# Optimization experiments

Hardware: AMD Instinct MI355X
Metric: run time of the kernel (lower is better)

The kernel has to match this reference:

```python
import jax, jax.numpy as jnp
import numpy as np


def _cross_head_proj(x, sw, qw1, qw2, kw1, kw2, qdd, kdd):
    # x: [B,N,T,S] attention logits/probs; sw: [N,N]
    # qw1/qw2: [B,T,I,N], kw1/kw2: [B,S,I,N] (I=2 dynamic rank), qdd: [B,T,N], kdd: [B,S,N]
    out = x + jnp.einsum('bnts,nm->bmts', x, sw)
    # low-rank dynamic mixing along query positions (sum over i reproduces the range(2) loop)
    qh = jnp.einsum('bnts,btin->bits', x, qw1)          # [B,I,T,S]
    out = out + jnp.einsum('bits,btin->bnts', qh, qw2)
    # low-rank dynamic mixing along key positions
    kh = jnp.einsum('bnts,bsin->bits', x, kw1)          # [B,I,T,S]
    out = out + jnp.einsum('bits,bsin->bnts', kh, kw2)
    # diagonal (per-head) dynamic terms
    out = out + x * jnp.transpose(qdd, (0, 2, 1))[:, :, :, None]   # [B,N,T,1]
    out = out + x * jnp.transpose(kdd, (0, 2, 1))[:, :, None, :]   # [B,N,1,S]
    return out


def setup_inputs() -> dict:
    key = jax.random.key(0)
    ks = jax.random.split(key, 18)
    B, N, T, S, D, I = 1, 32, 1024, 1024, 128, 2
    scale = 0.05  # dynamic weights come out of tanh/RMSnorm in the original; keep them small
    query = jax.random.normal(ks[0], (B, N, T, D), jnp.float32) * (D ** -0.5)
    k_ = jax.random.normal(ks[1], (B, N, S, D), jnp.float32)
    v_ = jax.random.normal(ks[2], (B, N, S, D), jnp.float32)
    neg = jnp.finfo(jnp.float32).min * 0.5  # matches make_causal_mask
    atten_mask = jnp.where(jnp.arange(S)[None, :] <= jnp.arange(T)[:, None], 0.0, neg).astype(jnp.float32)
    def dws(i0):
        return (
            jax.random.normal(ks[i0 + 0], (N, N), jnp.float32) * scale,
            jax.random.normal(ks[i0 + 1], (B, T, I, N), jnp.float32) * scale,
            jax.random.normal(ks[i0 + 2], (B, T, I, N), jnp.float32) * scale,
            jax.random.normal(ks[i0 + 3], (B, S, I, N), jnp.float32) * scale,
            jax.random.normal(ks[i0 + 4], (B, S, I, N), jnp.float32) * scale,
            jax.random.normal(ks[i0 + 5], (B, T, N), jnp.float32) * scale,
            jax.random.normal(ks[i0 + 6], (B, S, N), jnp.float32) * scale,
        )
    sw_pre, qw1_pre, qw2_pre, kw1_pre, kw2_pre, qdd_pre, kdd_pre = dws(3)
    sw_post, qw1_post, qw2_post, kw1_post, kw2_post, qdd_post, kdd_post = dws(10)
    return {
        'query': query, 'key': k_, 'value': v_, 'atten_mask': atten_mask,
        'sw_pre': sw_pre, 'qw1_pre': qw1_pre, 'qw2_pre': qw2_pre, 'kw1_pre': kw1_pre,
        'kw2_pre': kw2_pre, 'qdd_pre': qdd_pre, 'kdd_pre': kdd_pre,
        'sw_post': sw_post, 'qw1_post': qw1_post, 'qw2_post': qw2_post, 'kw1_post': kw1_post,
        'kw2_post': kw2_post, 'qdd_post': qdd_post, 'kdd_post': kdd_post,
    }


def reference(query, key, value, atten_mask,
              sw_pre, qw1_pre, qw2_pre, kw1_pre, kw2_pre, qdd_pre, kdd_pre,
              sw_post, qw1_post, qw2_post, kw1_post, kw2_post, qdd_post, kdd_post):
    # _atten_context: QK^T -> pre cross-head proj -> mask -> softmax -> post cross-head proj -> AV
    logits = jnp.einsum('bntd,bnsd->bnts', query, key)
    logits = _cross_head_proj(logits, sw_pre, qw1_pre, qw2_pre, kw1_pre, kw2_pre, qdd_pre, kdd_pre)
    logits = logits + atten_mask  # [T,S] broadcasts over [B,N,T,S]
    probs = jax.nn.softmax(logits, axis=-1)
    probs = _cross_head_proj(probs, sw_post, qw1_post, qw2_post, kw1_post, kw2_post, qdd_post, kdd_post)
    return jnp.einsum('bnts,bnsd->bntd', probs, value)
```

## Files before the change

kernel.cpp:

```cpp
#include <hip/hip_runtime.h>
#include <hip/hip_bf16.h>
#include <cstdint>
#include <cstddef>

#define T_DIM 1024
#define S_DIM 1024
#define N_HEADS 32
#define D_HEAD 128

typedef __attribute__((ext_vector_type(8))) short short8;
typedef __attribute__((ext_vector_type(4))) float floatx4;

__device__ inline int pack_bf16(float a, float b) {
    __hip_bfloat162 h = __float22bfloat162_rn(make_float2(a, b));
    int r; __builtin_memcpy(&r, &h, 4); return r;
}
__device__ inline ushort f2b(float x) {
    __hip_bfloat16 h = __float2bfloat16(x);
    ushort u; __builtin_memcpy(&u, &h, 2); return u;
}
__device__ inline float b2f(ushort u) {
    unsigned int v = ((unsigned int)u) << 16;
    float f; __builtin_memcpy(&f, &v, 4); return f;
}

__global__ __launch_bounds__(256) void tobf16(const float* __restrict__ Q,
                                              const float* __restrict__ K,
                                              ushort* __restrict__ Qb,
                                              ushort* __restrict__ Kb) {
    const size_t gid = (size_t)blockIdx.x * 256 + threadIdx.x;
    #pragma unroll
    for (int j = 0; j < 2; ++j) {
        size_t i = gid + (size_t)j * 524288;
        float4 q = ((const float4*)Q)[i];
        int2 qp; qp.x = pack_bf16(q.x, q.y); qp.y = pack_bf16(q.z, q.w);
        ((int2*)Qb)[i] = qp;
        float4 k = ((const float4*)K)[i];
        int2 kp; kp.x = pack_bf16(k.x, k.y); kp.y = pack_bf16(k.z, k.w);
        ((int2*)Kb)[i] = kp;
    }
}

__global__ __launch_bounds__(256) void vt_kernel(const float* __restrict__ V,
                                                 ushort* __restrict__ Vt) {
    const int s0 = blockIdx.x * 64;
    const int n  = blockIdx.y;
    __shared__ float lds[128 * 65];

    const int tid = threadIdx.x;
    const float* Vn = V + ((size_t)n * S_DIM + s0) * D_HEAD;

    #pragma unroll
    for (int it = 0; it < 8; ++it) {
        int idx = tid + it * 256;
        int d4 = idx & 31, s = idx >> 5;
        float4 v = *(const float4*)(Vn + (size_t)s * D_HEAD + d4 * 4);
        lds[(d4 * 4 + 0) * 65 + s] = v.x;
        lds[(d4 * 4 + 1) * 65 + s] = v.y;
        lds[(d4 * 4 + 2) * 65 + s] = v.z;
        lds[(d4 * 4 + 3) * 65 + s] = v.w;
    }
    __syncthreads();

    ushort* Vtn = Vt + (size_t)n * D_HEAD * S_DIM;
    #pragma unroll
    for (int it = 0; it < 4; ++it) {
        int idx = tid + it * 256;
        int sg = idx & 7, d = idx >> 3;
        const float* src = &lds[d * 65 + sg * 8];
        int4 o;
        o.x = pack_bf16(src[0], src[1]);
        o.y = pack_bf16(src[2], src[3]);
        o.z = pack_bf16(src[4], src[5]);
        o.w = pack_bf16(src[6], src[7]);
        *(int4*)&Vtn[(size_t)d * S_DIM + s0 + sg * 8] = o;
    }
}

__global__ __launch_bounds__(256, 2) void qk2(const ushort* __restrict__ Qb,
                                              const ushort* __restrict__ Kb,
                                              ushort* __restrict__ Lb) {
    const int bid  = blockIdx.x;
    const int xcd  = bid & 7;
    const int i    = bid >> 3;
    const int st   = i & 15;
    const int pair = (i >> 4) * 8 + xcd;
    const int n    = pair >> 4;
    const int tt   = pair & 15;
    if (st > tt) return;

    __shared__ int Qt[64 * 64];
    __shared__ int Kt[64 * 64];

    const int tid = threadIdx.x;
    const int wv = tid >> 6, ln = tid & 63;
    const int frow = ln & 15, quad = ln >> 4;

    const ushort* Qn = Qb + ((size_t)n * T_DIM + (size_t)tt * 64) * D_HEAD;
    const ushort* Kn = Kb + ((size_t)n * S_DIM + (size_t)st * 64) * D_HEAD;

    #pragma unroll
    for (int rep = 0; rep < 8; ++rep) {
        int idx = (tid + rep * 256) & 1023;
        int row = idx >> 4;
        int c   = idx & 15;
        int kb  = c >> 2, qw = c & 3;
        int dst = row * 64 + kb * 16 + ((qw * 4) ^ (4 * (row & 3)));
        if (rep < 4) {
            uint4 v = *(const uint4*)(Qn + (size_t)row * D_HEAD + c * 8);
            *(uint4*)&Qt[dst] = v;
        } else {
            uint4 v = *(const uint4*)(Kn + (size_t)row * D_HEAD + c * 8);
            *(uint4*)&Kt[dst] = v;
        }
    }
    __syncthreads();

    const int swz = 4 * (frow & 3);
    floatx4 acc[4] = {};
    #pragma unroll
    for (int kb = 0; kb < 4; ++kb) {
        const short8 af = *(const short8*)&Qt[(wv * 16 + frow) * 64 + kb * 16 + ((quad * 4) ^ swz)];
        #pragma unroll
        for (int si = 0; si < 4; ++si) {
            const short8 bf = *(const short8*)&Kt[(si * 16 + frow) * 64 + kb * 16 + ((quad * 4) ^ swz)];
            acc[si] = __builtin_amdgcn_mfma_f32_16x16x32_bf16(af, bf, acc[si], 0, 0, 0);
        }
    }
    __syncthreads();

    ushort* Ot = (ushort*)Qt;
    #pragma unroll
    for (int si = 0; si < 4; ++si)
        #pragma unroll
        for (int r = 0; r < 4; ++r)
            Ot[(wv * 16 + quad * 4 + r) * 72 + si * 16 + frow] = f2b(acc[si][r]);
    __syncthreads();

    #pragma unroll
    for (int it = 0; it < 2; ++it) {
        int idx = tid + it * 256;
        int row = idx >> 3, col = idx & 7;
        int4 v = *(const int4*)&Ot[row * 72 + col * 8];
        *(int4*)&Lb[((size_t)n * T_DIM + tt * 64 + row) * S_DIM + st * 64 + col * 8] = v;
    }
}

__global__ __launch_bounds__(256) void mat4_kernel(
        const float* __restrict__ sw_pre,  const float* __restrict__ qw1_pre,
        const float* __restrict__ qw2_pre, const float* __restrict__ qdd_pre,
        const float* __restrict__ kw1_pre, const float* __restrict__ kw2_pre,
        const float* __restrict__ kdd_pre,
        const float* __restrict__ sw_post,  const float* __restrict__ qw1_post,
        const float* __restrict__ qw2_post, const float* __restrict__ qdd_post,
        const float* __restrict__ kw1_post, const float* __restrict__ kw2_post,
        const float* __restrict__ kdd_post,
        ushort* __restrict__ mats) {
    const float *sw, *w1, *w2, *dd;
    float idadd;
    switch (blockIdx.y) {
        case 0:  sw = sw_pre;  w1 = qw1_pre;  w2 = qw2_pre;  dd = qdd_pre;  idadd = 1.0f; break;
        case 1:  sw = nullptr; w1 = kw1_pre;  w2 = kw2_pre;  dd = kdd_pre;  idadd = 0.0f; break;
        case 2:  sw = sw_post; w1 = qw1_post; w2 = qw2_post; dd = qdd_post; idadd = 1.0f; break;
        default: sw = nullptr; w1 = kw1_post; w2 = kw2_post; dd = kdd_post; idadd = 0.0f; break;
    }
    ushort* out = mats + (size_t)blockIdx.y * 1024 * 1024;

    const int t = blockIdx.x;
    const int tid = threadIdx.x;
    const int m = tid >> 3;
    const int n0 = (tid & 7) * 4;

    const float w2m0 = w2[t * 64 + m];
    const float w2m1 = w2[t * 64 + 32 + m];
    const float ddm  = dd[t * 32 + m];

    float v[4];
    #pragma unroll
    for (int j = 0; j < 4; ++j) {
        int n = n0 + j;
        float r = w1[t * 64 + n] * w2m0 + w1[t * 64 + 32 + n] * w2m1;
        if (sw) r += sw[n * 32 + m];
        if (n == m) r += idadd + ddm;
        v[j] = r;
    }
    int p0 = pack_bf16(v[0], v[1]);
    int p1 = pack_bf16(v[2], v[3]);
    int2 st = make_int2(p0, p1);
    *(int2*)&out[(size_t)t * 1024 + m * 32 + n0] = st;
}

__global__ __launch_bounds__(256) void rowstat(const ushort* __restrict__ Lb,
                                               float2* __restrict__ stats) {
    const int wv = threadIdx.x >> 6;
    const int ln = threadIdx.x & 63;
    const int r0 = blockIdx.x * 4 + wv;
    const int t  = r0 & (T_DIM - 1);
    const ushort* row = Lb + (size_t)r0 * S_DIM;

    float v[2][8];
    #pragma unroll
    for (int it = 0; it < 2; ++it) {
        const int i0 = it * 512 + ln * 8;
        #pragma unroll
        for (int j = 0; j < 8; ++j) v[it][j] = -INFINITY;
        if (i0 <= t) {
            uint4 raw = *(const uint4*)&row[i0];
            v[it][0] = b2f((ushort)(raw.x & 0xffff)); v[it][1] = b2f((ushort)(raw.x >> 16));
            v[it][2] = b2f((ushort)(raw.y & 0xffff)); v[it][3] = b2f((ushort)(raw.y >> 16));
            v[it][4] = b2f((ushort)(raw.z & 0xffff)); v[it][5] = b2f((ushort)(raw.z >> 16));
            v[it][6] = b2f((ushort)(raw.w & 0xffff)); v[it][7] = b2f((ushort)(raw.w >> 16));
            #pragma unroll
            for (int j = 0; j < 8; ++j)
                if (i0 + j > t) v[it][j] = -INFINITY;
        }
    }

    float m = -INFINITY;
    #pragma unroll
    for (int it = 0; it < 2; ++it)
        #pragma unroll
        for (int j = 0; j < 8; ++j) m = fmaxf(m, v[it][j]);
    #pragma unroll
    for (int off = 32; off > 0; off >>= 1) m = fmaxf(m, __shfl_xor(m, off));

    float ssum = 0.0f;
    #pragma unroll
    for (int it = 0; it < 2; ++it)
        #pragma unroll
        for (int j = 0; j < 8; ++j)
            ssum += (v[it][j] > -1e37f) ? __expf(v[it][j] - m) : 0.0f;
    #pragma unroll
    for (int off = 32; off > 0; off >>= 1) ssum += __shfl_xor(ssum, off);

    if (ln == 0) stats[r0] = make_float2(m, 1.0f / ssum);
}

template<bool SM>
__global__ __launch_bounds__(256, 4) void proj5(ushort* __restrict__ Lb,
                                                const ushort* __restrict__ Cmat,
                                                const ushort* __restrict__ Kmat,
                                                const float2* __restrict__ stats) {
    const int bid = blockIdx.y * 64 + blockIdx.x;
    const int xcd = bid & 7;
    const int idx = bid >> 3;
    const int ty  = ((idx >> 6) << 3) + xcd;
    const int sx  = idx & 63;

    const int s0 = sx * 16;
    const int t0 = ty * 16;
    if (s0 > t0 + 15) return;

    __shared__ __align__(16) ushort Xs[16 * 648];
    __shared__ __align__(16) float  Kp[16 * 260];

    const int tid = threadIdx.x;
    const int wv = tid >> 6, ln = tid & 63;
    const int frow = ln & 15, quad = ln >> 4;

    #pragma unroll
    for (int it = 0; it < 4; ++it) {
        int slot = tid + it * 256;
        int c    = slot & 1;
        int row  = slot >> 1;
        int nn   = row >> 4, tl = row & 15;
        uint4 ld = *(const uint4*)(Lb + ((size_t)nn * T_DIM + t0 + tl) * S_DIM + s0 + c * 8);
        ushort u[8];
        u[0] = (ushort)(ld.x & 0xffff);  u[1] = (ushort)(ld.x >> 16);
        u[2] = (ushort)(ld.y & 0xffff);  u[3] = (ushort)(ld.y >> 16);
        u[4] = (ushort)(ld.z & 0xffff);  u[5] = (ushort)(ld.z >> 16);
        u[6] = (ushort)(ld.w & 0xffff);  u[7] = (ushort)(ld.w >> 16);
        if (SM) {
            const float2 ms = stats[nn * T_DIM + t0 + tl];
            const int tG = t0 + tl, sbase = s0 + c * 8;
            #pragma unroll
            for (int j = 0; j < 8; ++j) {
                float x = (sbase + j <= tG) ? __expf(b2f(u[j]) - ms.x) * ms.y : 0.0f;
                u[j] = f2b(x);
            }
        }
        ushort* xp = &Xs[tl * 648 + (c * 8) * 40 + nn];
        #pragma unroll
        for (int j = 0; j < 8; ++j) xp[j * 40] = u[j];
    }
    __syncthreads();

    #pragma unroll
    for (int mh = 0; mh < 2; ++mh) {
        #pragma unroll
        for (int k = 0; k < 4; ++k) {
            const int sl = wv * 4 + k;
            const short8 af = *(const short8*)(Kmat + (size_t)(s0 + sl) * 1024 + (mh * 16 + frow) * 32 + quad * 8);
            const short8 bf = *(const short8*)&Xs[frow * 648 + sl * 40 + quad * 8];
            floatx4 z = {0.f, 0.f, 0.f, 0.f};
            floatx4 d = __builtin_amdgcn_mfma_f32_16x16x32_bf16(af, bf, z, 0, 0, 0);
            *(floatx4*)&Kp[frow * 260 + sl * 16 + quad * 4] = d;
        }
        __syncthreads();

        #pragma unroll
        for (int i = 0; i < 4; ++i) {
            const int tl = wv * 4 + i;
            const int tg = t0 + tl;
            const short8 bf = *(const short8*)(Cmat + (size_t)tg * 1024 + (mh * 16 + frow) * 32 + quad * 8);
            const short8 af = *(const short8*)&Xs[tl * 648 + frow * 40 + quad * 8];
            floatx4 z = {0.f, 0.f, 0.f, 0.f};
            floatx4 d = __builtin_amdgcn_mfma_f32_16x16x32_bf16(af, bf, z, 0, 0, 0);
            float v[4];
            #pragma unroll
            for (int r = 0; r < 4; ++r) {
                const int sl = quad * 4 + r;
                float val = d[r] + Kp[tl * 260 + sl * 16 + frow];
                v[r] = (s0 + sl > tg) ? 0.0f : val;
            }
            uint2 stv;
            stv.x = (unsigned)pack_bf16(v[0], v[1]);
            stv.y = (unsigned)pack_bf16(v[2], v[3]);
            *(uint2*)&Lb[((size_t)(mh * 16 + frow) * T_DIM + tg) * S_DIM + s0 + quad * 4] = stv;
        }
        __syncthreads();
    }
}

__global__ __launch_bounds__(256, 3) void av4(const ushort* __restrict__ P,
                                              const ushort* __restrict__ Vt,
                                              float* __restrict__ O) {
    const int tid = threadIdx.x;
    const int wv = tid >> 6, ln = tid & 63;
    const int frow = ln & 15, quad = ln >> 4;
    const int n  = blockIdx.x;
    const int tt = 31 - blockIdx.y;
    const int t0 = tt * 32;

    __shared__ ushort red[4][32][136];

    const ushort* Pn  = P  + ((size_t)n * T_DIM + t0) * S_DIM;
    const ushort* Vtn = Vt + (size_t)n * D_HEAD * S_DIM;

    const int nsteps  = tt + 1;
    const int nclean0 = t0 >> 5;
    const int nclean1 = (t0 + 16) >> 5;

    floatx4 acc[2][8] = {};
    for (int sb = wv; sb < nsteps; sb += 4) {
        const int scol = sb * 32 + quad * 8;
        short8 a0 = *(const short8*)(Pn + (size_t)frow * S_DIM + scol);
        short8 a1 = *(const short8*)(Pn + (size_t)(16 + frow) * S_DIM + scol);
        if (sb >= nclean0) {
            const int tg = t0 + frow;
            #pragma unroll
            for (int j = 0; j < 8; ++j)
                if (scol + j > tg) a0[j] = 0;
        }
        if (sb >= nclean1) {
            const int tg = t0 + 16 + frow;
            #pragma unroll
            for (int j = 0; j < 8; ++j)
                if (scol + j > tg) a1[j] = 0;
        }
        #pragma unroll
        for (int dc = 0; dc < 8; ++dc) {
            const short8 b = *(const short8*)(Vtn + (size_t)(dc * 16 + frow) * S_DIM + sb * 32 + quad * 8);
            acc[0][dc] = __builtin_amdgcn_mfma_f32_16x16x32_bf16(a0, b, acc[0][dc], 0, 0, 0);
            acc[1][dc] = __builtin_amdgcn_mfma_f32_16x16x32_bf16(a1, b, acc[1][dc], 0, 0, 0);
        }
    }

    #pragma unroll
    for (int tq = 0; tq < 2; ++tq)
        #pragma unroll
        for (int dc = 0; dc < 8; ++dc)
            #pragma unroll
            for (int r = 0; r < 4; ++r)
                red[wv][tq * 16 + quad * 4 + r][dc * 16 + frow] = f2b(acc[tq][dc][r]);
    __syncthreads();

    #pragma unroll
    for (int it = 0; it < 4; ++it) {
        int idx = tid + it * 256;
        int d4 = idx & 31, tr = idx >> 5;
        float4 v;
        v.x = b2f(red[0][tr][d4 * 4 + 0]) + b2f(red[1][tr][d4 * 4 + 0]) + b2f(red[2][tr][d4 * 4 + 0]) + b2f(red[3][tr][d4 * 4 + 0]);
        v.y = b2f(red[0][tr][d4 * 4 + 1]) + b2f(red[1][tr][d4 * 4 + 1]) + b2f(red[2][tr][d4 * 4 + 1]) + b2f(red[3][tr][d4 * 4 + 1]);
        v.z = b2f(red[0][tr][d4 * 4 + 2]) + b2f(red[1][tr][d4 * 4 + 2]) + b2f(red[2][tr][d4 * 4 + 2]) + b2f(red[3][tr][d4 * 4 + 2]);
        v.w = b2f(red[0][tr][d4 * 4 + 3]) + b2f(red[1][tr][d4 * 4 + 3]) + b2f(red[2][tr][d4 * 4 + 3]) + b2f(red[3][tr][d4 * 4 + 3]);
        *(float4*)&O[((size_t)n * T_DIM + t0 + tr) * D_HEAD + d4 * 4] = v;
    }
}

extern "C" void kernel_launch(void* const* d_in, const int* in_sizes, int n_in,
                              void* d_out, int out_size, void* d_ws, size_t ws_size,
                              hipStream_t stream) {
    const float* Q    = (const float*)d_in[0];
    const float* K    = (const float*)d_in[1];
    const float* V    = (const float*)d_in[2];
    const float* sw_pre  = (const float*)d_in[4];
    const float* qw1_pre = (const float*)d_in[5];
    const float* qw2_pre = (const float*)d_in[6];
    const float* kw1_pre = (const float*)d_in[7];
    const float* kw2_pre = (const float*)d_in[8];
    const float* qdd_pre = (const float*)d_in[9];
    const float* kdd_pre = (const float*)d_in[10];
    const float* sw_post  = (const float*)d_in[11];
    const float* qw1_post = (const float*)d_in[12];
    const float* qw2_post = (const float*)d_in[13];
    const float* kw1_post = (const float*)d_in[14];
    const float* kw2_post = (const float*)d_in[15];
    const float* qdd_post = (const float*)d_in[16];
    const float* kdd_post = (const float*)d_in[17];

    ushort* Lb = (ushort*)d_ws;
    ushort* Vt = (ushort*)((char*)d_ws + (size_t)64 * 1024 * 1024);
    ushort* Qb = (ushort*)((char*)d_ws + (size_t)72 * 1024 * 1024);
    ushort* Kb = (ushort*)((char*)d_ws + (size_t)80 * 1024 * 1024);
    float*  O  = (float*)d_out;

    ushort* mats  = (ushort*)d_out;
    ushort* Cpre  = mats + 0 * 1024 * 1024;
    ushort* Kpre  = mats + 1 * 1024 * 1024;
    ushort* Cpost = mats + 2 * 1024 * 1024;
    ushort* Kpost = mats + 3 * 1024 * 1024;
    float2* stats = (float2*)((char*)d_out + (size_t)8 * 1024 * 1024);

    mat4_kernel<<<dim3(1024, 4), 256, 0, stream>>>(
        sw_pre, qw1_pre, qw2_pre, qdd_pre, kw1_pre, kw2_pre, kdd_pre,
        sw_post, qw1_post, qw2_post, qdd_post, kw1_post, kw2_post, kdd_post, mats);
    tobf16<<<dim3(2048), 256, 0, stream>>>(Q, K, Qb, Kb);
    vt_kernel<<<dim3(16, 32), 256, 0, stream>>>(V, Vt);

    qk2<<<dim3(8192), 256, 0, stream>>>(Qb, Kb, Lb);
    proj5<false><<<dim3(64, 64), 256, 0, stream>>>(Lb, Cpre, Kpre, nullptr);
    rowstat<<<dim3(8192), 256, 0, stream>>>(Lb, stats);
    proj5<true><<<dim3(64, 64), 256, 0, stream>>>(Lb, Cpost, Kpost, stats);
    av4<<<dim3(32, 32), 256, 0, stream>>>(Lb, Vt, O);
}
```

Baseline: 246.0 us.

## Fuse softmax row statistics into pre-projection kernel with online partial reduction

Removes the separate rowstat pass that re-read the full bf16 logits tensor. The pre-projection kernel now computes per-tile partial max/sum-exp with an online-softmax merge and writes them to a small buffer. A lightweight statreduce kernel combines them into per-row stats, stored in [t][n] order. This trades a full logits read for extra shuffles/exps in proj and a smaller partial-stat buffer round-trip.

Result: no change. 244.6 us (-0.6%).

```diff
diff --git a/kernel.cpp b/kernel.cpp
--- a/kernel.cpp
+++ b/kernel.cpp
@@ -190,57 +190,12 @@
     *(int2*)&out[(size_t)t * 1024 + m * 32 + n0] = st;
 }
 
-__global__ __launch_bounds__(256) void rowstat(const ushort* __restrict__ Lb,
-                                               float2* __restrict__ stats) {
-    const int wv = threadIdx.x >> 6;
-    const int ln = threadIdx.x & 63;
-    const int r0 = blockIdx.x * 4 + wv;
-    const int t  = r0 & (T_DIM - 1);
-    const ushort* row = Lb + (size_t)r0 * S_DIM;
-
-    float v[2][8];
-    #pragma unroll
-    for (int it = 0; it < 2; ++it) {
-        const int i0 = it * 512 + ln * 8;
-        #pragma unroll
-        for (int j = 0; j < 8; ++j) v[it][j] = -INFINITY;
-        if (i0 <= t) {
-            uint4 raw = *(const uint4*)&row[i0];
-            v[it][0] = b2f((ushort)(raw.x & 0xffff)); v[it][1] = b2f((ushort)(raw.x >> 16));
-            v[it][2] = b2f((ushort)(raw.y & 0xffff)); v[it][3] = b2f((ushort)(raw.y >> 16));
-            v[it][4] = b2f((ushort)(raw.z & 0xffff)); v[it][5] = b2f((ushort)(raw.z >> 16));
-            v[it][6] = b2f((ushort)(raw.w & 0xffff)); v[it][7] = b2f((ushort)(raw.w >> 16));
-            #pragma unroll
-            for (int j = 0; j < 8; ++j)
-                if (i0 + j > t) v[it][j] = -INFINITY;
-        }
-    }
-
-    float m = -INFINITY;
-    #pragma unroll
-    for (int it = 0; it < 2; ++it)
-        #pragma unroll
-        for (int j = 0; j < 8; ++j) m = fmaxf(m, v[it][j]);
-    #pragma unroll
-    for (int off = 32; off > 0; off >>= 1) m = fmaxf(m, __shfl_xor(m, off));
-
-    float ssum = 0.0f;
-    #pragma unroll
-    for (int it = 0; it < 2; ++it)
-        #pragma unroll
-        for (int j = 0; j < 8; ++j)
-            ssum += (v[it][j] > -1e37f) ? __expf(v[it][j] - m) : 0.0f;
-    #pragma unroll
-    for (int off = 32; off > 0; off >>= 1) ssum += __shfl_xor(ssum, off);
-
-    if (ln == 0) stats[r0] = make_float2(m, 1.0f / ssum);
-}
-
 template<bool SM>
-__global__ __launch_bounds__(256, 4) void proj5(ushort* __restrict__ Lb,
+__global__ __launch_bounds__(256, 4) void proj6(ushort* __restrict__ Lb,
                                                 const ushort* __restrict__ Cmat,
                                                 const ushort* __restrict__ Kmat,
-                                                const float2* __restrict__ stats) {
+                                                const float2* __restrict__ stats2,
+                                                float2* __restrict__ pstat) {
     const int bid = blockIdx.y * 64 + blockIdx.x;
     const int xcd = bid & 7;
     const int idx = bid >> 3;
@@ -271,7 +226,7 @@
         u[4] = (ushort)(ld.z & 0xffff);  u[5] = (ushort)(ld.z >> 16);
         u[6] = (ushort)(ld.w & 0xffff);  u[7] = (ushort)(ld.w >> 16);
         if (SM) {
-            const float2 ms = stats[nn * T_DIM + t0 + tl];
+            const float2 ms = stats2[(t0 + tl) * 32 + nn];
             const int tG = t0 + tl, sbase = s0 + c * 8;
             #pragma unroll
             for (int j = 0; j < 8; ++j) {
@@ -307,11 +262,32 @@
             floatx4 z = {0.f, 0.f, 0.f, 0.f};
             floatx4 d = __builtin_amdgcn_mfma_f32_16x16x32_bf16(af, bf, z, 0, 0, 0);
             float v[4];
+            float lm = -INFINITY, lsum = 0.0f;
             #pragma unroll
             for (int r = 0; r < 4; ++r) {
                 const int sl = quad * 4 + r;
                 float val = d[r] + Kp[tl * 260 + sl * 16 + frow];
-                v[r] = (s0 + sl > tg) ? 0.0f : val;
+                const bool ok = (s0 + sl <= tg);
+                v[r] = ok ? val : 0.0f;
+                if (!SM) lm = fmaxf(lm, ok ? val : -INFINITY);
+            }
+            if (!SM) {
+                #pragma unroll
+                for (int r = 0; r < 4; ++r) {
+                    const int sl = quad * 4 + r;
+                    if (s0 + sl <= tg) lsum += __expf(v[r] - lm);
+                }
+                #pragma unroll
+                for (int off = 16; off <= 32; off <<= 1) {
+                    float om = __shfl_xor(lm, off);
+                    float os = __shfl_xor(lsum, off);
+                    float nm = fmaxf(lm, om);
+                    float a = (lm > -1e37f) ? lsum * __expf(lm - nm) : 0.0f;
+                    float b = (om > -1e37f) ? os   * __expf(om - nm) : 0.0f;
+                    lm = nm; lsum = a + b;
+                }
+                if (quad == 0)
+                    pstat[((size_t)tg * 64 + sx) * 32 + mh * 16 + frow] = make_float2(lm, lsum);
             }
             uint2 stv;
             stv.x = (unsigned)pack_bf16(v[0], v[1]);
@@ -320,6 +296,46 @@
         }
         __syncthreads();
     }
+}
+
+__global__ __launch_bounds__(256) void statreduce(const float2* __restrict__ pstat,
+                                                  float2* __restrict__ stats2) {
+    const int t = blockIdx.x;
+    const int ty = t >> 4;
+    const int total = (ty + 1) * 32;
+    __shared__ float sm[32][65];
+    __shared__ float ss[32][65];
+
+    const int tid = threadIdx.x;
+    for (int base = 0; base < total; base += 256) {
+        int idx = base + tid;
+        if (idx < total) {
+            float2 p = pstat[(size_t)t * 2048 + idx];
+            sm[idx & 31][idx >> 5] = p.x;
+            ss[idx & 31][idx >> 5] = p.y;
+        }
+    }
+    __syncthreads();
+
+    const int n = tid >> 3, j = tid & 7;
+    float m = -INFINITY, s = 0.0f;
+    for (int sx = j; sx <= ty; sx += 8) {
+        float om = sm[n][sx], os = ss[n][sx];
+        float nm = fmaxf(m, om);
+        float a = (m  > -1e37f) ? s  * __expf(m  - nm) : 0.0f;
+        float b = (om > -1e37f) ? os * __expf(om - nm) : 0.0f;
+        m = nm; s = a + b;
+    }
+    #pragma unroll
+    for (int off = 1; off < 8; off <<= 1) {
+        float om = __shfl_xor(m, off);
+        float os = __shfl_xor(s, off);
+        float nm = fmaxf(m, om);
+        float a = (m  > -1e37f) ? s  * __expf(m  - nm) : 0.0f;
+        float b = (om > -1e37f) ? os * __expf(om - nm) : 0.0f;
+        m = nm; s = a + b;
+    }
+    if (j == 0) stats2[t * 32 + n] = make_float2(m, 1.0f / s);
 }
 
 __global__ __launch_bounds__(256, 3) void av4(const ushort* __restrict__ P,
@@ -413,6 +429,7 @@
     ushort* Vt = (ushort*)((char*)d_ws + (size_t)64 * 1024 * 1024);
     ushort* Qb = (ushort*)((char*)d_ws + (size_t)72 * 1024 * 1024);
     ushort* Kb = (ushort*)((char*)d_ws + (size_t)80 * 1024 * 1024);
+    float2* pstat = (float2*)((char*)d_ws + (size_t)96 * 1024 * 1024);
     float*  O  = (float*)d_out;
 
     ushort* mats  = (ushort*)d_out;
@@ -420,7 +437,7 @@
     ushort* Kpre  = mats + 1 * 1024 * 1024;
     ushort* Cpost = mats + 2 * 1024 * 1024;
     ushort* Kpost = mats + 3 * 1024 * 1024;
-    float2* stats = (float2*)((char*)d_out + (size_t)8 * 1024 * 1024);
+    float2* stats2 = (float2*)((char*)d_out + (size_t)8 * 1024 * 1024);
 
     mat4_kernel<<<dim3(1024, 4), 256, 0, stream>>>(
         sw_pre, qw1_pre, qw2_pre, qdd_pre, kw1_pre, kw2_pre, kdd_pre,
@@ -429,8 +446,8 @@
     vt_kernel<<<dim3(16, 32), 256, 0, stream>>>(V, Vt);
 
     qk2<<<dim3(8192), 256, 0, stream>>>(Qb, Kb, Lb);
-    proj5<false><<<dim3(64, 64), 256, 0, stream>>>(Lb, Cpre, Kpre, nullptr);
-    rowstat<<<dim3(8192), 256, 0, stream>>>(Lb, stats);
-    proj5<true><<<dim3(64, 64), 256, 0, stream>>>(Lb, Cpost, Kpost, stats);
+    proj6<false><<<dim3(64, 64), 256, 0, stream>>>(Lb, Cpre, Kpre, nullptr, pstat);
+    statreduce<<<dim3(1024), 256, 0, stream>>>(pstat, stats2);
+    proj6<true><<<dim3(64, 64), 256, 0, stream>>>(Lb, Cpost, Kpost, stats2, nullptr);
     av4<<<dim3(32, 32), 256, 0, stream>>>(Lb, Vt, O);
 }
```
